# Kernel optimization log

Hardware: AMD Instinct MI355X
Metric: run time of the kernel (lower is better)

Reference implementation:

```python
import jax, jax.numpy as jnp
import numpy as np

B, C, CI, H, W = 8, 256, 64, 64, 64  # batch, in_channels, inter_channels, spatial


def conv1x1(x, w, b):
    # x: [B,C,H,W], w: [O,C] (1x1 kernel), b: [O]
    return jnp.einsum('bchw,oc->bohw', x, w) + b[None, :, None, None]


def setup_inputs() -> dict:
    key = jax.random.key(0)
    ks = jax.random.split(key, 9)
    s_in = 1.0 / np.sqrt(C)
    s_ci = 1.0 / np.sqrt(CI)
    return {
        'x': jax.random.normal(ks[0], (B, C, H, W), dtype=jnp.float32),
        'g_w': jax.random.uniform(ks[1], (CI, C), jnp.float32, -s_in, s_in),
        'g_b': jax.random.uniform(ks[2], (CI,), jnp.float32, -s_in, s_in),
        'theta_w': jax.random.uniform(ks[3], (CI, C), jnp.float32, -s_in, s_in),
        'theta_b': jax.random.uniform(ks[4], (CI,), jnp.float32, -s_in, s_in),
        'phi_w': jax.random.uniform(ks[5], (CI, C), jnp.float32, -s_in, s_in),
        'phi_b': jax.random.uniform(ks[6], (CI,), jnp.float32, -s_in, s_in),
        'w_w': jax.random.uniform(ks[7], (C, CI), jnp.float32, -s_ci, s_ci),
        'w_b': jax.random.uniform(ks[8], (C,), jnp.float32, -s_ci, s_ci),
    }


def reference(x, g_w, g_b, theta_w, theta_b, phi_w, phi_b, w_w, w_b):
    b, c, h, w = x.shape
    n = h * w
    # 1x1 conv projections, flattened over spatial positions -> [B, N, CI]
    g_x = conv1x1(x, g_w, g_b).reshape(b, CI, n).transpose(0, 2, 1)
    theta_x = conv1x1(x, theta_w, theta_b).reshape(b, CI, n).transpose(0, 2, 1)
    phi_x = conv1x1(x, phi_w, phi_b).reshape(b, CI, n)  # [B, CI, N]
    # Full non-scaled attention over spatial positions
    f = jnp.einsum('bnc,bcm->bnm', theta_x, phi_x)       # [B, N, N]
    f_div_c = jax.nn.softmax(f, axis=-1)
    y = jnp.einsum('bnm,bmc->bnc', f_div_c, g_x)         # [B, N, CI]
    y = y.transpose(0, 2, 1).reshape(b, CI, h, w)
    w_y = conv1x1(y, w_w, w_b)                            # [B, C, H, W]
    return w_y + x
```

## Files before the change

### kernel.cpp

```cpp
#include <hip/hip_runtime.h>
#include <hip/hip_bf16.h>

#define B_  8
#define C_  256
#define CI_ 64
#define N_  4096

typedef short short8 __attribute__((ext_vector_type(8)));
typedef float floatx4 __attribute__((ext_vector_type(4)));

__device__ __forceinline__ unsigned short f2bf(float f) {
    unsigned u = __builtin_bit_cast(unsigned, f);
    u += 0x7FFFu + ((u >> 16) & 1u);
    return (unsigned short)(u >> 16);
}
__device__ __forceinline__ ushort4 f4tobf(float4 v) {
    ushort4 r; r.x = f2bf(v.x); r.y = f2bf(v.y); r.z = f2bf(v.z); r.w = f2bf(v.w);
    return r;
}

__global__ __launch_bounds__(256) void proj_kernel(
    const float* __restrict__ x,
    const float* __restrict__ wg, const float* __restrict__ bg,
    const float* __restrict__ wt, const float* __restrict__ bt,
    const float* __restrict__ wp, const float* __restrict__ bp,
    unsigned short* __restrict__ gws,
    unsigned short* __restrict__ tws,
    unsigned short* __restrict__ pws)
{
    constexpr int WS = 40;
    constexpr int GS = 72;
    __shared__ __align__(16) unsigned short ws[192 * WS];
    __shared__ __align__(16) unsigned short gt[64 * GS];

    const int t    = threadIdx.x;
    const int lane = t & 63;
    const int w    = t >> 6;
    const int l15  = lane & 15;
    const int quad = lane >> 4;
    const int n0   = blockIdx.x * 64;
    const int b    = blockIdx.y;

    floatx4 acc[12];
#pragma unroll
    for (int ot = 0; ot < 12; ++ot) { floatx4 z = {0.f, 0.f, 0.f, 0.f}; acc[ot] = z; }

    const int nA = n0 + w * 16 + l15;

    for (int kk = 0; kk < 8; ++kk) {
        if (kk) __syncthreads();
#pragma unroll
        for (int it = 0; it < 6; ++it) {
            int u = t + it * 256;
            int row = u >> 3, c4 = u & 7;
            const float* src = (row < 64)  ? (wg + row * C_)
                             : (row < 128) ? (wt + (row - 64) * C_)
                                           : (wp + (row - 128) * C_);
            float4 v = *(const float4*)(src + kk * 32 + c4 * 4);
            *(ushort4*)&ws[row * WS + c4 * 4] = f4tobf(v);
        }
        __syncthreads();

        short8 af;
        const float* xcol = x + ((size_t)(b * C_ + kk * 32 + quad * 8)) * N_ + nA;
#pragma unroll
        for (int j = 0; j < 8; ++j)
            af[j] = (short)f2bf(xcol[(size_t)j * N_]);

#pragma unroll
        for (int ot = 0; ot < 12; ++ot) {
            short8 bf = *(const short8*)&ws[(ot * 16 + l15) * WS + quad * 8];
            acc[ot] = __builtin_amdgcn_mfma_f32_16x16x32_bf16(af, bf, acc[ot], 0, 0, 0);
        }
    }

#pragma unroll
    for (int ot = 0; ot < 12; ++ot) {
        const int oc = ot * 16 + l15;
        const float bias = (ot < 4) ? bg[oc] : (ot < 8) ? bt[oc - 64] : bp[oc - 128];
        if (ot < 4) {
#pragma unroll
            for (int r = 0; r < 4; ++r)
                gt[oc * GS + w * 16 + quad * 4 + r] = f2bf(acc[ot][r] + bias);
        } else {
            unsigned short* dst = (ot < 8) ? tws : pws;
            const int ci = (ot < 8) ? (oc - 64) : (oc - 128);
#pragma unroll
            for (int r = 0; r < 4; ++r) {
                int n = n0 + w * 16 + quad * 4 + r;
                dst[((size_t)b * N_ + n) * CI_ + ci] = f2bf(acc[ot][r] + bias);
            }
        }
    }
    __syncthreads();
#pragma unroll
    for (int it = 0; it < 2; ++it) {
        int u = t + it * 256;
        int ci = u >> 3, n8 = u & 7;
        uint4 v = *(const uint4*)&gt[ci * GS + n8 * 8];
        *(uint4*)(gws + ((size_t)b * CI_ + ci) * N_ + n0 + n8 * 8) = v;
    }
}

__global__ __launch_bounds__(256) void attn_kernel(
    const unsigned short* __restrict__ gws,
    const unsigned short* __restrict__ tws,
    const unsigned short* __restrict__ pws,
    unsigned short* __restrict__ yws)
{
    constexpr int LDW = 72;
    __shared__ __align__(16) unsigned short Ks[2][64 * LDW];
    __shared__ __align__(16) unsigned short Vs[2][64 * LDW];
    __shared__ __align__(16) unsigned short Ps[64 * LDW];

    const int t    = threadIdx.x;
    const int lane = t & 63;
    const int w    = t >> 6;
    const int l15  = lane & 15;
    const int quad = lane >> 4;
    const int b    = blockIdx.x;
    const int q0   = blockIdx.y * 64;

    const int srow = t >> 3;
    const int sc8  = t & 7;

    {
        const uint4* qsrc = (const uint4*)(tws + ((size_t)b * N_ + q0) * CI_);
        const uint4* ksrc = (const uint4*)(pws + ((size_t)b * N_) * CI_);
#pragma unroll
        for (int it = 0; it < 2; ++it) {
            int u = t + it * 256;
            int row = u >> 3, c8 = u & 7;
            uint4 qv = qsrc[u];
            uint4 kv = ksrc[u];
            uint4 vv = *(const uint4*)(gws + ((size_t)b * CI_ + row) * N_ + c8 * 8);
            *(uint4*)&Ps[row * LDW + c8 * 8]    = qv;
            *(uint4*)&Ks[0][row * LDW + c8 * 8] = kv;
            *(uint4*)&Vs[0][row * LDW + c8 * 8] = vv;
        }
    }
    __syncthreads();

    short8 qf[2];
#pragma unroll
    for (int ks = 0; ks < 2; ++ks)
        qf[ks] = *(const short8*)&Ps[(w * 16 + l15) * LDW + ks * 32 + quad * 8];

    short8 ones;
#pragma unroll
    for (int j = 0; j < 8; ++j) ones[j] = (short)0x3F80;

    floatx4 Oacc[4], lacc;
    { floatx4 z = {0.f, 0.f, 0.f, 0.f}; lacc = z;
#pragma unroll
      for (int f = 0; f < 4; ++f) Oacc[f] = z; }

    const uint4* kbase = (const uint4*)(pws + (size_t)b * N_ * CI_);
    const unsigned short* vbase = gws + ((size_t)b * CI_ + srow) * N_ + sc8 * 8;

    for (int j = 0; j < N_ / 64; ++j) {
        const int p = j & 1;

        const int jn = (j + 1) & 63;
        uint4 pk0 = kbase[jn * 512 + t];
        uint4 pk1 = kbase[jn * 512 + t + 256];
        uint4 pv0 = *(const uint4*)(vbase + jn * 64);
        uint4 pv1 = *(const uint4*)(vbase + 32 * N_ + jn * 64);

        floatx4 s[4];
#pragma unroll
        for (int f = 0; f < 4; ++f) {
            floatx4 z = {0.f, 0.f, 0.f, 0.f};
            s[f] = z;
#pragma unroll
            for (int ks = 0; ks < 2; ++ks) {
                short8 kb = *(const short8*)&Ks[p][(f * 16 + l15) * LDW + ks * 32 + quad * 8];
                s[f] = __builtin_amdgcn_mfma_f32_16x16x32_bf16(qf[ks], kb, s[f], 0, 0, 0);
            }
        }

        const float LOG2E = 1.4426950408889634f;
#pragma unroll
        for (int r = 0; r < 4; ++r)
#pragma unroll
            for (int f = 0; f < 4; ++f)
                Ps[(w * 16 + quad * 4 + r) * LDW + f * 16 + l15] =
                    f2bf(exp2f(s[f][r] * LOG2E));

#pragma unroll
        for (int ks = 0; ks < 2; ++ks) {
            short8 pa = *(const short8*)&Ps[(w * 16 + l15) * LDW + ks * 32 + quad * 8];
            lacc = __builtin_amdgcn_mfma_f32_16x16x32_bf16(pa, ones, lacc, 0, 0, 0);
#pragma unroll
            for (int f = 0; f < 4; ++f) {
                short8 vb = *(const short8*)&Vs[p][(f * 16 + l15) * LDW + ks * 32 + quad * 8];
                Oacc[f] = __builtin_amdgcn_mfma_f32_16x16x32_bf16(pa, vb, Oacc[f], 0, 0, 0);
            }
        }

        *(uint4*)&Ks[1 - p][srow * LDW + sc8 * 8]        = pk0;
        *(uint4*)&Ks[1 - p][(srow + 32) * LDW + sc8 * 8] = pk1;
        *(uint4*)&Vs[1 - p][srow * LDW + sc8 * 8]        = pv0;
        *(uint4*)&Vs[1 - p][(srow + 32) * LDW + sc8 * 8] = pv1;

        __syncthreads();
    }

#pragma unroll
    for (int r = 0; r < 4; ++r) {
        float inv = 1.f / lacc[r];
        int row = q0 + w * 16 + quad * 4 + r;
#pragma unroll
        for (int f = 0; f < 4; ++f)
            yws[((size_t)b * N_ + row) * CI_ + f * 16 + l15] = f2bf(Oacc[f][r] * inv);
    }
}

__global__ __launch_bounds__(256) void out_kernel(
    const unsigned short* __restrict__ yws,
    const float* __restrict__ ww,
    const float* __restrict__ wb,
    const float* __restrict__ x,
    float* __restrict__ out)
{
    constexpr int WS = 72;
    __shared__ __align__(16) unsigned short wws[C_ * WS];

    const int t    = threadIdx.x;
    const int lane = t & 63;
    const int w    = t >> 6;
    const int l15  = lane & 15;
    const int quad = lane >> 4;
    const int n0   = blockIdx.x * 64;
    const int b    = blockIdx.y;

#pragma unroll
    for (int it = 0; it < 16; ++it) {
        int u = t + it * 256;
        int row = u >> 4, c4 = u & 15;
        float4 v = *(const float4*)(ww + row * CI_ + c4 * 4);
        *(ushort4*)&wws[row * WS + c4 * 4] = f4tobf(v);
    }
    __syncthreads();

    floatx4 acc[16];
#pragma unroll
    for (int ot = 0; ot < 16; ++ot) { floatx4 z = {0.f, 0.f, 0.f, 0.f}; acc[ot] = z; }

    const int nB = n0 + w * 16 + l15;
#pragma unroll
    for (int ks = 0; ks < 2; ++ks) {
        short8 bfrag = *(const short8*)(yws + ((size_t)b * N_ + nB) * CI_ + ks * 32 + quad * 8);
#pragma unroll
        for (int ot = 0; ot < 16; ++ot) {
            short8 afrag = *(const short8*)&wws[(ot * 16 + l15) * WS + ks * 32 + quad * 8];
            acc[ot] = __builtin_amdgcn_mfma_f32_16x16x32_bf16(afrag, bfrag, acc[ot], 0, 0, 0);
        }
    }

#pragma unroll
    for (int ot = 0; ot < 16; ++ot) {
#pragma unroll
        for (int r = 0; r < 4; ++r) {
            int c = ot * 16 + quad * 4 + r;
            size_t idx = ((size_t)b * C_ + c) * N_ + n0 + w * 16 + l15;
            out[idx] = acc[ot][r] + wb[c] + x[idx];
        }
    }
}

extern "C" void kernel_launch(void* const* d_in, const int* in_sizes, int n_in,
                              void* d_out, int out_size, void* d_ws, size_t ws_size,
                              hipStream_t stream) {
    const float* x  = (const float*)d_in[0];
    const float* gw = (const float*)d_in[1];
    const float* gb = (const float*)d_in[2];
    const float* tw = (const float*)d_in[3];
    const float* tb = (const float*)d_in[4];
    const float* pw = (const float*)d_in[5];
    const float* pb = (const float*)d_in[6];
    const float* ww = (const float*)d_in[7];
    const float* wb = (const float*)d_in[8];
    float* out = (float*)d_out;

    char* ws = (char*)d_ws;
    unsigned short* gws = (unsigned short*)(ws);
    unsigned short* tws = (unsigned short*)(ws + (4  << 20));
    unsigned short* pws = (unsigned short*)(ws + (8  << 20));
    unsigned short* yws = (unsigned short*)(ws + (12 << 20));

    proj_kernel<<<dim3(64, 8), 256, 0, stream>>>(x, gw, gb, tw, tb, pw, pb, gws, tws, pws);
    attn_kernel<<<dim3(8, 64), 256, 0, stream>>>(gws, tws, pws, yws);
    out_kernel<<<dim3(64, 8), 256, 0, stream>>>(yws, ww, wb, x, out);
}
```

Before: 219.3 us.

## Split attention over keys, keep P in registers, pipeline projection loads

The attention kernel now splits the key dimension in two across a third grid axis and writes unnormalized fp32 partial outputs and row sums, which the output kernel combines and normalizes. The S computation is transposed so the exp'd scores feed the PV product straight from registers through 16x16x16 MFMAs, removing the LDS round trip for P. The projection kernel double-buffers weight tiles and prefetches x, and conversions use packed bf16 instructions. The changes aim to raise occupancy and remove LDS traffic, at the cost of extra fp32 workspace traffic and a reduction step.

```diff
diff --git a/kernel.cpp b/kernel.cpp
--- a/kernel.cpp
+++ b/kernel.cpp
@@ -5,8 +5,11 @@
 #define C_  256
 #define CI_ 64
 #define N_  4096
-
-typedef short short8 __attribute__((ext_vector_type(8)));
+#define KSPLIT 2
+#define KTILES (N_ / 64 / KSPLIT)
+
+typedef short short8  __attribute__((ext_vector_type(8)));
+typedef short sh4     __attribute__((ext_vector_type(4)));
 typedef float floatx4 __attribute__((ext_vector_type(4)));
 
 __device__ __forceinline__ unsigned short f2bf(float f) {
@@ -14,9 +17,27 @@
     u += 0x7FFFu + ((u >> 16) & 1u);
     return (unsigned short)(u >> 16);
 }
-__device__ __forceinline__ ushort4 f4tobf(float4 v) {
-    ushort4 r; r.x = f2bf(v.x); r.y = f2bf(v.y); r.z = f2bf(v.z); r.w = f2bf(v.w);
-    return r;
+
+__device__ __forceinline__ unsigned pk2(float a, float b) {
+#if __has_builtin(__builtin_amdgcn_cvt_pk_bf16_f32)
+    auto r = __builtin_amdgcn_cvt_pk_bf16_f32(a, b);
+    return __builtin_bit_cast(unsigned, r);
+#else
+    return (unsigned)f2bf(a) | ((unsigned)f2bf(b) << 16);
+#endif
+}
+
+__device__ __forceinline__ floatx4 mfma32(short8 a, short8 b, floatx4 c) {
+    return __builtin_amdgcn_mfma_f32_16x16x32_bf16(a, b, c, 0, 0, 0);
+}
+__device__ __forceinline__ floatx4 mfma16(sh4 a, sh4 b, floatx4 c) {
+#if __has_builtin(__builtin_amdgcn_mfma_f32_16x16x16bf16_1k)
+    return __builtin_amdgcn_mfma_f32_16x16x16bf16_1k(a, b, c, 0, 0, 0);
+#else
+    floatx4 d;
+    asm("v_mfma_f32_16x16x16_bf16 %0, %1, %2, %3" : "=v"(d) : "v"(a), "v"(b), "v"(c));
+    return d;
+#endif
 }
 
 __global__ __launch_bounds__(256) void proj_kernel(
@@ -30,7 +51,7 @@
 {
     constexpr int WS = 40;
     constexpr int GS = 72;
-    __shared__ __align__(16) unsigned short ws[192 * WS];
+    __shared__ __align__(16) unsigned short wsl[2][192 * WS];
     __shared__ __align__(16) unsigned short gt[64 * GS];
 
     const int t    = threadIdx.x;
@@ -46,32 +67,55 @@
     for (int ot = 0; ot < 12; ++ot) { floatx4 z = {0.f, 0.f, 0.f, 0.f}; acc[ot] = z; }
 
     const int nA = n0 + w * 16 + l15;
+    const float* xbase = x + (size_t)b * C_ * N_ + nA;
+
+#pragma unroll
+    for (int it = 0; it < 6; ++it) {
+        int u = t + it * 256;
+        int row = u >> 3, c4 = u & 7;
+        const float* src = (row < 64)  ? (wg + row * C_)
+                         : (row < 128) ? (wt + (row - 64) * C_)
+                                       : (wp + (row - 128) * C_);
+        float4 v = *(const float4*)(src + c4 * 4);
+        uint2 uu = { pk2(v.x, v.y), pk2(v.z, v.w) };
+        *(uint2*)&wsl[0][row * WS + c4 * 4] = uu;
+    }
+    float xv[8];
+#pragma unroll
+    for (int j = 0; j < 8; ++j) xv[j] = xbase[(size_t)(quad * 8 + j) * N_];
+    __syncthreads();
 
     for (int kk = 0; kk < 8; ++kk) {
-        if (kk) __syncthreads();
-#pragma unroll
-        for (int it = 0; it < 6; ++it) {
-            int u = t + it * 256;
-            int row = u >> 3, c4 = u & 7;
-            const float* src = (row < 64)  ? (wg + row * C_)
-                             : (row < 128) ? (wt + (row - 64) * C_)
-                                           : (wp + (row - 128) * C_);
-            float4 v = *(const float4*)(src + kk * 32 + c4 * 4);
-            *(ushort4*)&ws[row * WS + c4 * 4] = f4tobf(v);
+        uint4 au = { pk2(xv[0], xv[1]), pk2(xv[2], xv[3]),
+                     pk2(xv[4], xv[5]), pk2(xv[6], xv[7]) };
+        short8 af = __builtin_bit_cast(short8, au);
+
+        float nx[8];
+        if (kk < 7) {
+#pragma unroll
+            for (int j = 0; j < 8; ++j)
+                nx[j] = xbase[(size_t)((kk + 1) * 32 + quad * 8 + j) * N_];
+#pragma unroll
+            for (int it = 0; it < 6; ++it) {
+                int u = t + it * 256;
+                int row = u >> 3, c4 = u & 7;
+                const float* src = (row < 64)  ? (wg + row * C_)
+                                 : (row < 128) ? (wt + (row - 64) * C_)
+                                               : (wp + (row - 128) * C_);
+                float4 v = *(const float4*)(src + (kk + 1) * 32 + c4 * 4);
+                uint2 uu = { pk2(v.x, v.y), pk2(v.z, v.w) };
+                *(uint2*)&wsl[(kk + 1) & 1][row * WS + c4 * 4] = uu;
+            }
+        }
+
+#pragma unroll
+        for (int ot = 0; ot < 12; ++ot) {
+            short8 bf = *(const short8*)&wsl[kk & 1][(ot * 16 + l15) * WS + quad * 8];
+            acc[ot] = mfma32(af, bf, acc[ot]);
         }
         __syncthreads();
-
-        short8 af;
-        const float* xcol = x + ((size_t)(b * C_ + kk * 32 + quad * 8)) * N_ + nA;
-#pragma unroll
-        for (int j = 0; j < 8; ++j)
-            af[j] = (short)f2bf(xcol[(size_t)j * N_]);
-
-#pragma unroll
-        for (int ot = 0; ot < 12; ++ot) {
-            short8 bf = *(const short8*)&ws[(ot * 16 + l15) * WS + quad * 8];
-            acc[ot] = __builtin_amdgcn_mfma_f32_16x16x32_bf16(af, bf, acc[ot], 0, 0, 0);
-        }
+#pragma unroll
+        for (int j = 0; j < 8; ++j) xv[j] = nx[j];
     }
 
 #pragma unroll
@@ -102,16 +146,16 @@
     }
 }
 
-__global__ __launch_bounds__(256) void attn_kernel(
+__global__ __launch_bounds__(256, 4) void attn_kernel(
     const unsigned short* __restrict__ gws,
     const unsigned short* __restrict__ tws,
     const unsigned short* __restrict__ pws,
-    unsigned short* __restrict__ yws)
+    float* __restrict__ Opart,
+    float* __restrict__ lpart)
 {
     constexpr int LDW = 72;
     __shared__ __align__(16) unsigned short Ks[2][64 * LDW];
     __shared__ __align__(16) unsigned short Vs[2][64 * LDW];
-    __shared__ __align__(16) unsigned short Ps[64 * LDW];
 
     const int t    = threadIdx.x;
     const int lane = t & 63;
@@ -120,48 +164,49 @@
     const int quad = lane >> 4;
     const int b    = blockIdx.x;
     const int q0   = blockIdx.y * 64;
+    const int sp   = blockIdx.z;
 
     const int srow = t >> 3;
     const int sc8  = t & 7;
 
+    const uint4* kbase = (const uint4*)(pws + ((size_t)b * N_ + sp * (N_ / KSPLIT)) * CI_);
+    const unsigned short* vbase =
+        gws + ((size_t)b * CI_ + srow) * N_ + sp * (N_ / KSPLIT) + sc8 * 8;
+
+    short8 qf[2];
     {
-        const uint4* qsrc = (const uint4*)(tws + ((size_t)b * N_ + q0) * CI_);
-        const uint4* ksrc = (const uint4*)(pws + ((size_t)b * N_) * CI_);
-#pragma unroll
-        for (int it = 0; it < 2; ++it) {
-            int u = t + it * 256;
-            int row = u >> 3, c8 = u & 7;
-            uint4 qv = qsrc[u];
-            uint4 kv = ksrc[u];
-            uint4 vv = *(const uint4*)(gws + ((size_t)b * CI_ + row) * N_ + c8 * 8);
-            *(uint4*)&Ps[row * LDW + c8 * 8]    = qv;
-            *(uint4*)&Ks[0][row * LDW + c8 * 8] = kv;
-            *(uint4*)&Vs[0][row * LDW + c8 * 8] = vv;
-        }
+        const unsigned short* qrow = tws + ((size_t)b * N_ + q0 + w * 16 + l15) * CI_;
+        qf[0] = *(const short8*)(qrow + quad * 8);
+        qf[1] = *(const short8*)(qrow + 32 + quad * 8);
+    }
+
+    {
+        uint4 k0 = kbase[t];
+        uint4 k1 = kbase[t + 256];
+        uint4 v0 = *(const uint4*)(vbase);
+        uint4 v1 = *(const uint4*)(vbase + 32 * N_);
+        *(uint4*)&Ks[0][srow * LDW + sc8 * 8]        = k0;
+        *(uint4*)&Ks[0][(srow + 32) * LDW + sc8 * 8] = k1;
+        *(uint4*)&Vs[0][srow * LDW + sc8 * 8]        = v0;
+        *(uint4*)&Vs[0][(srow + 32) * LDW + sc8 * 8] = v1;
     }
     __syncthreads();
 
-    short8 qf[2];
-#pragma unroll
-    for (int ks = 0; ks < 2; ++ks)
-        qf[ks] = *(const short8*)&Ps[(w * 16 + l15) * LDW + ks * 32 + quad * 8];
-
-    short8 ones;
-#pragma unroll
-    for (int j = 0; j < 8; ++j) ones[j] = (short)0x3F80;
+    sh4 ones4;
+#pragma unroll
+    for (int j = 0; j < 4; ++j) ones4[j] = (short)0x3F80;
 
     floatx4 Oacc[4], lacc;
     { floatx4 z = {0.f, 0.f, 0.f, 0.f}; lacc = z;
 #pragma unroll
       for (int f = 0; f < 4; ++f) Oacc[f] = z; }
 
-    const uint4* kbase = (const uint4*)(pws + (size_t)b * N_ * CI_);
-    const unsigned short* vbase = gws + ((size_t)b * CI_ + srow) * N_ + sc8 * 8;
-
-    for (int j = 0; j < N_ / 64; ++j) {
-        const int p = j & 1;
-
-        const int jn = (j + 1) & 63;
+    const float LOG2E = 1.4426950408889634f;
+
+    for (int j = 0; j < KTILES; ++j) {
+        const int p  = j & 1;
+        const int jn = (j + 1) & (KTILES - 1);
+
         uint4 pk0 = kbase[jn * 512 + t];
         uint4 pk1 = kbase[jn * 512 + t + 256];
         uint4 pv0 = *(const uint4*)(vbase + jn * 64);
@@ -174,27 +219,28 @@
             s[f] = z;
 #pragma unroll
             for (int ks = 0; ks < 2; ++ks) {
-                short8 kb = *(const short8*)&Ks[p][(f * 16 + l15) * LDW + ks * 32 + quad * 8];
-                s[f] = __builtin_amdgcn_mfma_f32_16x16x32_bf16(qf[ks], kb, s[f], 0, 0, 0);
+                short8 ka = *(const short8*)&Ks[p][(f * 16 + l15) * LDW + ks * 32 + quad * 8];
+                s[f] = mfma32(ka, qf[ks], s[f]);
             }
         }
 
-        const float LOG2E = 1.4426950408889634f;
-#pragma unroll
-        for (int r = 0; r < 4; ++r)
-#pragma unroll
-            for (int f = 0; f < 4; ++f)
-                Ps[(w * 16 + quad * 4 + r) * LDW + f * 16 + l15] =
-                    f2bf(exp2f(s[f][r] * LOG2E));
-
-#pragma unroll
-        for (int ks = 0; ks < 2; ++ks) {
-            short8 pa = *(const short8*)&Ps[(w * 16 + l15) * LDW + ks * 32 + quad * 8];
-            lacc = __builtin_amdgcn_mfma_f32_16x16x32_bf16(pa, ones, lacc, 0, 0, 0);
-#pragma unroll
-            for (int f = 0; f < 4; ++f) {
-                short8 vb = *(const short8*)&Vs[p][(f * 16 + l15) * LDW + ks * 32 + quad * 8];
-                Oacc[f] = __builtin_amdgcn_mfma_f32_16x16x32_bf16(pa, vb, Oacc[f], 0, 0, 0);
+        sh4 pfr[4];
+#pragma unroll
+        for (int f = 0; f < 4; ++f) {
+            uint2 uu = { pk2(__builtin_amdgcn_exp2f(s[f][0] * LOG2E),
+                             __builtin_amdgcn_exp2f(s[f][1] * LOG2E)),
+                         pk2(__builtin_amdgcn_exp2f(s[f][2] * LOG2E),
+                             __builtin_amdgcn_exp2f(s[f][3] * LOG2E)) };
+            pfr[f] = __builtin_bit_cast(sh4, uu);
+        }
+
+#pragma unroll
+        for (int f = 0; f < 4; ++f) {
+            lacc = mfma16(pfr[f], ones4, lacc);
+#pragma unroll
+            for (int fc = 0; fc < 4; ++fc) {
+                sh4 vb = *(const sh4*)&Vs[p][(fc * 16 + l15) * LDW + f * 16 + quad * 4];
+                Oacc[fc] = mfma16(pfr[f], vb, Oacc[fc]);
             }
         }
 
@@ -208,16 +254,19 @@
 
 #pragma unroll
     for (int r = 0; r < 4; ++r) {
-        float inv = 1.f / lacc[r];
         int row = q0 + w * 16 + quad * 4 + r;
-#pragma unroll
-        for (int f = 0; f < 4; ++f)
-            yws[((size_t)b * N_ + row) * CI_ + f * 16 + l15] = f2bf(Oacc[f][r] * inv);
+        size_t obase = ((size_t)(sp * B_ + b) * N_ + row) * CI_;
+#pragma unroll
+        for (int fc = 0; fc < 4; ++fc)
+            Opart[obase + fc * 16 + l15] = Oacc[fc][r];
+        if (l15 == 0)
+            lpart[(size_t)(sp * B_ + b) * N_ + row] = lacc[r];
     }
 }
 
 __global__ __launch_bounds__(256) void out_kernel(
-    const unsigned short* __restrict__ yws,
+    const float* __restrict__ Opart,
+    const float* __restrict__ lpart,
     const float* __restrict__ ww,
     const float* __restrict__ wb,
     const float* __restrict__ x,
@@ -239,7 +288,8 @@
         int u = t + it * 256;
         int row = u >> 4, c4 = u & 15;
         float4 v = *(const float4*)(ww + row * CI_ + c4 * 4);
-        *(ushort4*)&wws[row * WS + c4 * 4] = f4tobf(v);
+        uint2 uu = { pk2(v.x, v.y), pk2(v.z, v.w) };
+        *(uint2*)&wws[row * WS + c4 * 4] = uu;
     }
     __syncthreads();
 
@@ -248,13 +298,26 @@
     for (int ot = 0; ot < 16; ++ot) { floatx4 z = {0.f, 0.f, 0.f, 0.f}; acc[ot] = z; }
 
     const int nB = n0 + w * 16 + l15;
+    const float l0 = lpart[(size_t)b * N_ + nB];
+    const float l1 = lpart[(size_t)(B_ + b) * N_ + nB];
+    const float inv = 1.f / (l0 + l1);
+
 #pragma unroll
     for (int ks = 0; ks < 2; ++ks) {
-        short8 bfrag = *(const short8*)(yws + ((size_t)b * N_ + nB) * CI_ + ks * 32 + quad * 8);
+        const float4* o0 = (const float4*)(Opart + ((size_t)b * N_ + nB) * CI_ + ks * 32 + quad * 8);
+        const float4* o1 = (const float4*)(Opart + ((size_t)(B_ + b) * N_ + nB) * CI_ + ks * 32 + quad * 8);
+        float4 a0 = o0[0], a1 = o0[1];
+        float4 b0 = o1[0], b1 = o1[1];
+        float y0 = (a0.x + b0.x) * inv, y1 = (a0.y + b0.y) * inv;
+        float y2 = (a0.z + b0.z) * inv, y3 = (a0.w + b0.w) * inv;
+        float y4 = (a1.x + b1.x) * inv, y5 = (a1.y + b1.y) * inv;
+        float y6 = (a1.z + b1.z) * inv, y7 = (a1.w + b1.w) * inv;
+        uint4 bu = { pk2(y0, y1), pk2(y2, y3), pk2(y4, y5), pk2(y6, y7) };
+        short8 bfrag = __builtin_bit_cast(short8, bu);
 #pragma unroll
         for (int ot = 0; ot < 16; ++ot) {
             short8 afrag = *(const short8*)&wws[(ot * 16 + l15) * WS + ks * 32 + quad * 8];
-            acc[ot] = __builtin_amdgcn_mfma_f32_16x16x32_bf16(afrag, bfrag, acc[ot], 0, 0, 0);
+            acc[ot] = mfma32(afrag, bfrag, acc[ot]);
         }
     }
 
@@ -284,12 +347,13 @@
     float* out = (float*)d_out;
 
     char* ws = (char*)d_ws;
-    unsigned short* gws = (unsigned short*)(ws);
-    unsigned short* tws = (unsigned short*)(ws + (4  << 20));
-    unsigned short* pws = (unsigned short*)(ws + (8  << 20));
-    unsigned short* yws = (unsigned short*)(ws + (12 << 20));
+    unsigned short* gws   = (unsigned short*)(ws);
+    unsigned short* tws   = (unsigned short*)(ws + (4  << 20));
+    unsigned short* pws   = (unsigned short*)(ws + (8  << 20));
+    float*          Opart = (float*)        (ws + (12 << 20));
+    float*          lpart = (float*)        (ws + (28 << 20));
 
     proj_kernel<<<dim3(64, 8), 256, 0, stream>>>(x, gw, gb, tw, tb, pw, pb, gws, tws, pws);
-    attn_kernel<<<dim3(8, 64), 256, 0, stream>>>(gws, tws, pws, yws);
-    out_kernel<<<dim3(64, 8), 256, 0, stream>>>(yws, ww, wb, x, out);
-}
+    attn_kernel<<<dim3(8, 64, KSPLIT), 256, 0, stream>>>(gws, tws, pws, Opart, lpart);
+    out_kernel<<<dim3(64, 8), 256, 0, stream>>>(Opart, lpart, ww, wb, x, out);
+}
```

After: 198.3 us. 9.6% less time.
